# Optimization experiments

Hardware: AMD Instinct MI355X
Metric: run time of the kernel (lower is better)

The kernel has to match this reference:

```python
import jax, jax.numpy as jnp
import numpy as np

EMBED_DIM = 1024
HEAD_DIM = 64


def setup_inputs() -> dict:
    key = jax.random.key(0)
    ks = jax.random.split(key, 9)
    B, S, E, H = 4, 2048, EMBED_DIM, HEAD_DIM
    s = 1.0 / np.sqrt(E)
    return {
        "query": jax.random.normal(ks[0], (B, S, E), dtype=jnp.float32),
        "key": jax.random.normal(ks[1], (B, S, E), dtype=jnp.float32),
        "value": jax.random.normal(ks[2], (B, S, E), dtype=jnp.float32),
        "Wq": jax.random.normal(ks[3], (E, H), dtype=jnp.float32) * s,
        "bq": jnp.zeros((H,), dtype=jnp.float32),
        "Wk": jax.random.normal(ks[4], (E, H), dtype=jnp.float32) * s,
        "bk": jnp.zeros((H,), dtype=jnp.float32),
        "Wv": jax.random.normal(ks[5], (E, H), dtype=jnp.float32) * s,
        "bv": jnp.zeros((H,), dtype=jnp.float32),
    }


def reference(query, key, value, Wq, bq, Wk, bk, Wv, bv):
    # per-head linear projections: [B,S,E] @ [E,H] -> [B,S,H]
    q = jnp.einsum("bse,eh->bsh", query, Wq) + bq
    k = jnp.einsum("bse,eh->bsh", key, Wk) + bk
    v = jnp.einsum("bse,eh->bsh", value, Wv) + bv
    # NOTE: original code computes dim_k but never scales -> unscaled scores
    scores = jnp.einsum("bqh,bkh->bqk", q, k)  # [B,S,S]
    weights = jax.nn.softmax(scores, axis=-1)
    return jnp.einsum("bqk,bkh->bqh", weights, v)  # [B,S,H]
```

## Files before the change

### kernel.cpp

```cpp
#include <hip/hip_runtime.h>
#include <math.h>

#define B 4
#define S 2048
#define E 1024
#define H 64
#define BS (B*S)
#define LOG2E 1.44269504088896f
#define CINIT (-69.2493662f)

typedef float v4f __attribute__((ext_vector_type(4)));
typedef short v8s __attribute__((ext_vector_type(8)));
typedef unsigned short u16;
typedef u16 u16x8 __attribute__((ext_vector_type(8)));
typedef u16 u16x4 __attribute__((ext_vector_type(4)));

#define MFMA(a,b,c) __builtin_amdgcn_mfma_f32_16x16x32_bf16(a,b,c,0,0,0)

#define BARRIER_L() do { \
    asm volatile("s_waitcnt lgkmcnt(0)" ::: "memory"); \
    __builtin_amdgcn_s_barrier(); \
} while (0)

__device__ inline u16 rh_bf16(float x){ return (u16)((__float_as_uint(x)+0x8000u)>>16); }

__global__ __launch_bounds__(256) void wsetup_kernel(
    const float* __restrict__ Wq, const float* __restrict__ Wk,
    const float* __restrict__ Wv,
    u16* __restrict__ Wt_hi, u16* __restrict__ Wt_lo)
{
    __shared__ float wt[64][65];
    const int t  = threadIdx.x;
    const int p  = blockIdx.x >> 4;
    const int e0 = (blockIdx.x & 15) * 64;
    const float* Wsrc = (p==0) ? Wq : (p==1 ? Wk : Wv);
    const float scale = (p==0) ? LOG2E : 1.0f;

    #pragma unroll
    for (int i=0;i<16;i++){
        int e_l = i*4 + (t>>6);
        wt[e_l][t&63] = Wsrc[(size_t)(e0+e_l)*H + (t&63)] * scale;
    }
    __syncthreads();

    const int h = t>>2, e16 = (t&3)*16;
    u16 hi_a[16], lo_a[16];
    #pragma unroll
    for (int j=0;j<16;j++){
        float f = wt[e16+j][h];
        unsigned u = __float_as_uint(f);
        hi_a[j] = (u16)(u>>16);
        float hif = __uint_as_float(u & 0xFFFF0000u);
        lo_a[j] = rh_bf16(f - hif);
    }
    u16* dh = Wt_hi + (size_t)(p*64+h)*E + e0 + e16;
    u16* dl = Wt_lo + (size_t)(p*64+h)*E + e0 + e16;
    *(u16x8*)dh     = *(u16x8*)&hi_a[0];
    *(u16x8*)(dh+8) = *(u16x8*)&hi_a[8];
    *(u16x8*)dl     = *(u16x8*)&lo_a[0];
    *(u16x8*)(dl+8) = *(u16x8*)&lo_a[8];
}

__global__ __launch_bounds__(256) void proj_kernel(
    const float* __restrict__ query, const float* __restrict__ key_,
    const float* __restrict__ value,
    const u16* __restrict__ Wt_hi, const u16* __restrict__ Wt_lo,
    const float* __restrict__ bq, const float* __restrict__ bk,
    const float* __restrict__ bv,
    u16* __restrict__ q_hi, u16* __restrict__ q_lo,
    u16* __restrict__ k_hi, u16* __restrict__ k_lo,
    u16* __restrict__ vt)
{
    __shared__ __align__(16) u16 xh[32][72], xl[32][72];
    __shared__ __align__(16) u16 wh[64][72], wl[64][72];
    __shared__ __align__(16) u16 vtile[64][40];

    const int t  = threadIdx.x;
    const int p  = blockIdx.x >> 8;
    const int r0 = (blockIdx.x & 255) * 32;
    const float* xp = (p==0) ? query : (p==1 ? key_ : value);
    const int wv = t>>6, lane = t&63, m = lane&15, quad = lane>>4;
    const int whalf = wv>>1, nh = wv&1;

    const int srow = t>>3, se8 = (t&7)*8;
    const int swh  = t>>2, seo  = (t&3)*16;

    const float* xb  = xp + (size_t)(r0+srow)*E + se8;
    const u16*   shb = Wt_hi + (size_t)(p*64+swh)*E + seo;
    const u16*   slb = Wt_lo + (size_t)(p*64+swh)*E + seo;

    v4f acc[2];
    acc[0] = (v4f){0.f,0.f,0.f,0.f};
    acc[1] = (v4f){0.f,0.f,0.f,0.f};

    float4 xA[2], xB[2];
    u16x8  wA[4], wB[4];
    xA[0] = *(const float4*)(xb);
    xA[1] = *(const float4*)(xb+4);
    wA[0] = *(const u16x8*)(shb);     wA[1] = *(const u16x8*)(shb+8);
    wA[2] = *(const u16x8*)(slb);     wA[3] = *(const u16x8*)(slb+8);
    xB[0] = *(const float4*)(xb+64);
    xB[1] = *(const float4*)(xb+68);
    wB[0] = *(const u16x8*)(shb+64);  wB[1] = *(const u16x8*)(shb+72);
    wB[2] = *(const u16x8*)(slb+64);  wB[3] = *(const u16x8*)(slb+72);

#define PROJ_ITER(EC, XC, WC, PREF)                                            \
    {                                                                          \
        BARRIER_L();                                                           \
        float fv[8] = {XC[0].x,XC[0].y,XC[0].z,XC[0].w,                        \
                       XC[1].x,XC[1].y,XC[1].z,XC[1].w};                       \
        u16 ha[8], la[8];                                                      \
        _Pragma("unroll")                                                      \
        for (int j=0;j<8;j++){                                                 \
            unsigned u = __float_as_uint(fv[j]);                               \
            ha[j] = (u16)(u>>16);                                              \
            la[j] = rh_bf16(fv[j] - __uint_as_float(u & 0xFFFF0000u));         \
        }                                                                      \
        *(u16x8*)&xh[srow][se8] = *(u16x8*)&ha[0];                             \
        *(u16x8*)&xl[srow][se8] = *(u16x8*)&la[0];                             \
        *(u16x8*)&wh[swh][seo]   = WC[0];                                      \
        *(u16x8*)&wh[swh][seo+8] = WC[1];                                      \
        *(u16x8*)&wl[swh][seo]   = WC[2];                                      \
        *(u16x8*)&wl[swh][seo+8] = WC[3];                                      \
        if (PREF){                                                             \
            const float* xn = xb + ((EC)+2)*64;                                \
            XC[0] = *(const float4*)(xn);                                      \
            XC[1] = *(const float4*)(xn+4);                                    \
            const u16* shn = shb + ((EC)+2)*64;                                \
            const u16* sln = slb + ((EC)+2)*64;                                \
            WC[0]=*(const u16x8*)(shn); WC[1]=*(const u16x8*)(shn+8);          \
            WC[2]=*(const u16x8*)(sln); WC[3]=*(const u16x8*)(sln+8);          \
        }                                                                      \
        BARRIER_L();                                                           \
        v8s ah0 = *(v8s*)&xh[whalf*16+m][quad*8];                              \
        v8s ah1 = *(v8s*)&xh[whalf*16+m][32+quad*8];                           \
        v8s al0 = *(v8s*)&xl[whalf*16+m][quad*8];                              \
        v8s al1 = *(v8s*)&xl[whalf*16+m][32+quad*8];                           \
        _Pragma("unroll")                                                      \
        for (int i=0;i<2;i++){                                                 \
            const int nt = nh*2+i;                                             \
            v8s bh0 = *(v8s*)&wh[nt*16+m][quad*8];                             \
            v8s bh1 = *(v8s*)&wh[nt*16+m][32+quad*8];                          \
            v8s bl0 = *(v8s*)&wl[nt*16+m][quad*8];                             \
            v8s bl1 = *(v8s*)&wl[nt*16+m][32+quad*8];                          \
            v4f d = acc[i];                                                    \
            d = MFMA(ah0,bh0,d); d = MFMA(ah1,bh1,d);                          \
            d = MFMA(al0,bh0,d); d = MFMA(al1,bh1,d);                          \
            d = MFMA(ah0,bl0,d); d = MFMA(ah1,bl1,d);                          \
            acc[i] = d;                                                        \
        }                                                                      \
    }

    for (int ec2=0; ec2<16; ec2+=2){
        PROJ_ITER(ec2,   xA, wA, (ec2+2<16))
        PROJ_ITER(ec2+1, xB, wB, (ec2+3<16))
    }
#undef PROJ_ITER

    const float* bp = (p==0) ? bq : (p==1 ? bk : bv);
    if (p<2){
        const float bscale = (p==0) ? LOG2E : 1.0f;
        u16* dh = (p==0) ? q_hi : k_hi;
        u16* dl = (p==0) ? q_lo : k_lo;
        #pragma unroll
        for (int i=0;i<2;i++){
            const int hl = (nh*2+i)*16+m;
            const float bb = bp[hl]*bscale;
            #pragma unroll
            for (int r=0;r<4;r++){
                const int gr = r0 + whalf*16 + quad*4 + r;
                const float val = acc[i][r] + bb;
                unsigned u = __float_as_uint(val);
                u16 hi = (u16)(u>>16);
                float hif = __uint_as_float(u & 0xFFFF0000u);
                u16 lo = rh_bf16(val - hif);
                dh[(size_t)gr*H + hl] = hi;
                dl[(size_t)gr*H + hl] = lo;
            }
        }
    } else {
        const int rlb = whalf*16 + quad*4;
        #pragma unroll
        for (int i=0;i<2;i++){
            const int hl = (nh*2+i)*16+m;
            const float bb = bp[hl];
            u16 vv[4];
            #pragma unroll
            for (int r=0;r<4;r++) vv[r] = rh_bf16(acc[i][r] + bb);
            *(u16x4*)&vtile[hl][rlb] = *(u16x4*)&vv[0];
        }
        __syncthreads();
        const int h = t>>2, so = (t&3)*8;
        const int bidx = r0 >> 11, s0l = r0 & (S-1);
        u16* dst = vt + ((size_t)(bidx*H + h))*S + s0l + so;
        *(u16x8*)dst = *(const u16x8*)&vtile[h][so];
    }
}

__global__ __launch_bounds__(256) void attn_kernel(
    const u16* __restrict__ qh_g, const u16* __restrict__ ql_g,
    const u16* __restrict__ kh_g, const u16* __restrict__ kl_g,
    const u16* __restrict__ vt_g,
    float* __restrict__ accw, float* __restrict__ lw, int ksplit)
{
    __shared__ __align__(16) u16 khe[2][16][72];
    __shared__ __align__(16) u16 kle[2][16][72];
    __shared__ __align__(16) u16 vtl[64][40];
    __shared__ __align__(16) u16 pl[4][16][40];

    const int t = threadIdx.x;
    const int wv = t>>6, lane = t&63, m = lane&15, quad = lane>>4;
    const int bid = blockIdx.x;
    const int qb = bid / ksplit, chunk = bid % ksplit;
    const int b = qb >> 5, s0 = (qb & 31)*64;
    const int ck = S / ksplit;
    const int j0base = chunk * ck;
    const int iters = ck / 32;

    const u16* qr = qh_g + (size_t)(b*S + s0 + wv*16 + m)*H + quad*8;
    const u16* qrl = ql_g + (size_t)(b*S + s0 + wv*16 + m)*H + quad*8;
    const v8s qh0 = *(const v8s*)(qr),  qh1 = *(const v8s*)(qr+32);
    const v8s ql0 = *(const v8s*)(qrl), ql1 = *(const v8s*)(qrl+32);

    v4f oacc[4];
    #pragma unroll
    for (int nt=0;nt<4;nt++) oacc[nt] = (v4f){0.f,0.f,0.f,0.f};
    float lp[4] = {0.f,0.f,0.f,0.f};
    const v4f cinit = (v4f){CINIT,CINIT,CINIT,CINIT};

    const int sj = t>>3, sh8 = (t&7)*8;
    const u16* khs = kh_g + (size_t)(b*S + j0base + sj)*H + sh8;
    const u16* kls = kl_g + (size_t)(b*S + j0base + sj)*H + sh8;
    u16* khd = &khe[sj&1][sj>>1][sh8];
    u16* kld = &kle[sj&1][sj>>1][sh8];
    const int vh = t>>2, vj8 = (t&3)*8;
    const u16* vts = vt_g + (size_t)(b*H + vh)*S + j0base + vj8;
    u16* vtd = &vtl[vh][vj8];

    u16x8 khA, klA, vtA, khB, klB, vtB;
    khA = *(const u16x8*)khs;
    klA = *(const u16x8*)kls;
    vtA = *(const u16x8*)vts;
    khB = *(const u16x8*)(khs + (size_t)32*H);
    klB = *(const u16x8*)(kls + (size_t)32*H);
    vtB = *(const u16x8*)(vts + 32);

#define ATTN_ITER(IT, KHC, KLC, VTC, PREF)                                     \
    {                                                                          \
        BARRIER_L();                                                           \
        *(u16x8*)khd = KHC; *(u16x8*)kld = KLC; *(u16x8*)vtd = VTC;            \
        if (PREF){                                                             \
            KHC = *(const u16x8*)(khs + (size_t)((IT)+2)*32*H);                \
            KLC = *(const u16x8*)(kls + (size_t)((IT)+2)*32*H);                \
            VTC = *(const u16x8*)(vts + ((IT)+2)*32);                          \
        }                                                                      \
        BARRIER_L();                                                           \
                \
        v4f sc[2];                                                             \
        _Pragma("unroll")                                                      \
        for (int jt=0;jt<2;jt++){                                              \
            const u16* kr  = &khe[jt][m][quad*8];                              \
            const u16* krl = &kle[jt][m][quad*8];                              \
            v8s b0 = *(const v8s*)kr,  b1 = *(const v8s*)(kr+32);              \
            v8s c0 = *(const v8s*)krl, c1 = *(const v8s*)(krl+32);             \
            v4f d = cinit;                                                     \
            d = MFMA(qh0,b0,d); d = MFMA(qh1,b1,d);                            \
            d = MFMA(ql0,b0,d); d = MFMA(ql1,b1,d);                            \
            d = MFMA(qh0,c0,d); d = MFMA(qh1,c1,d);                            \
            sc[jt] = d;                                                        \
        }                                                                      \
            \
        _Pragma("unroll")                                                      \
        for (int r=0;r<4;r++){                                                 \
            float p0 = exp2f(sc[0][r]);                     \
            float p1 = exp2f(sc[1][r]);                     \
            lp[r] += p0 + p1;                                                  \
            unsigned pk = ((__float_as_uint(p0)+0x8000u)>>16)                  \
                        | ((__float_as_uint(p1)+0x8000u) & 0xFFFF0000u);       \
            *(unsigned*)&pl[wv][quad*4+r][2*m] = pk;                           \
        }                                                                      \
          \
        v8s pa = *(const v8s*)&pl[wv][m][quad*8];                              \
        _Pragma("unroll")                                                      \
        for (int nt=0;nt<4;nt++){                                              \
            v8s vb = *(const v8s*)&vtl[nt*16+m][quad*8];                       \
            oacc[nt] = MFMA(pa, vb, oacc[nt]);                                 \
        }                                                                      \
    }

    for (int it=0; it<iters; it+=2){
        ATTN_ITER(it,   khA,klA,vtA, (it+2<iters))
        ATTN_ITER(it+1, khB,klB,vtB, (it+3<iters))
    }
#undef ATTN_ITER

    #pragma unroll
    for (int r=0;r<4;r++){
        float v = lp[r];
        v += __shfl_xor(v,1); v += __shfl_xor(v,2);
        v += __shfl_xor(v,4); v += __shfl_xor(v,8);
        lp[r] = v;
    }
    const int growb = b*S + s0 + wv*16;
    if (m==0){
        float4 lv; lv.x=lp[0]; lv.y=lp[1]; lv.z=lp[2]; lv.w=lp[3];
        *(float4*)(lw + (size_t)chunk*BS + growb + quad*4) = lv;
    }
    float* ab = accw + ((size_t)chunk*BS + growb)*H;
    #pragma unroll
    for (int nt=0;nt<4;nt++){
        #pragma unroll
        for (int r=0;r<4;r++)
            ab[(size_t)(quad*4+r)*H + nt*16 + m] = oacc[nt][r];
    }
}

__global__ __launch_bounds__(256) void merge_kernel(
    const float* __restrict__ accw, const float* __restrict__ lw,
    float* __restrict__ out, int ksplit)
{
    const int idx = blockIdx.x*256 + threadIdx.x;
    const int row = idx >> 4, h4 = (idx & 15)*4;
    float4 a = {0.f,0.f,0.f,0.f};
    float ls = 0.f;
    for (int c=0;c<ksplit;c++){
        const float4 t4 = *(const float4*)(accw + ((size_t)c*BS + row)*H + h4);
        a.x+=t4.x; a.y+=t4.y; a.z+=t4.z; a.w+=t4.w;
        ls += lw[(size_t)c*BS + row];
    }
    const float inv = __builtin_amdgcn_rcpf(ls);
    float4 o; o.x=a.x*inv; o.y=a.y*inv; o.z=a.z*inv; o.w=a.w*inv;
    *(float4*)(out + (size_t)row*H + h4) = o;
}

extern "C" void kernel_launch(void* const* d_in, const int* in_sizes, int n_in,
                              void* d_out, int out_size, void* d_ws, size_t ws_size,
                              hipStream_t stream) {
    const float* query = (const float*)d_in[0];
    const float* key_  = (const float*)d_in[1];
    const float* value = (const float*)d_in[2];
    const float* Wq    = (const float*)d_in[3];
    const float* bq    = (const float*)d_in[4];
    const float* Wk    = (const float*)d_in[5];
    const float* bk    = (const float*)d_in[6];
    const float* Wv    = (const float*)d_in[7];
    const float* bv    = (const float*)d_in[8];
    float* out = (float*)d_out;

    char* base = (char*)d_ws;
    size_t off = 0;
    u16* Wt_hi = (u16*)(base + off); off += (size_t)3*64*E*2;
    u16* Wt_lo = (u16*)(base + off); off += (size_t)3*64*E*2;
    u16* q_hi  = (u16*)(base + off); off += (size_t)BS*H*2;
    u16* q_lo  = (u16*)(base + off); off += (size_t)BS*H*2;
    u16* k_hi  = (u16*)(base + off); off += (size_t)BS*H*2;
    u16* k_lo  = (u16*)(base + off); off += (size_t)BS*H*2;
    u16* vt    = (u16*)(base + off); off += (size_t)BS*H*2;
    const size_t fixed = off;
    const size_t CH = (size_t)BS*H*4 + (size_t)BS*4;

    int K = 1;
    if      (ws_size >= fixed + 8*CH) K = 8;
    else if (ws_size >= fixed + 4*CH) K = 4;
    else if (ws_size >= fixed + 2*CH) K = 2;

    float* lw   = (float*)(base + fixed);
    float* accw = (float*)(base + fixed + (size_t)K*BS*4);

    wsetup_kernel<<<48, 256, 0, stream>>>(Wq, Wk, Wv, Wt_hi, Wt_lo);
    proj_kernel<<<768, 256, 0, stream>>>(query, key_, value, Wt_hi, Wt_lo,
                                         bq, bk, bv, q_hi, q_lo, k_hi, k_lo, vt);
    attn_kernel<<<128*K, 256, 0, stream>>>(q_hi, q_lo, k_hi, k_lo, vt, accw, lw, K);
    merge_kernel<<<512, 256, 0, stream>>>(accw, lw, out, K);
}
```

Before: 170.1 us.

## Prepack weights in MFMA fragment order and drop LDS staging in projection

The weight setup kernel now writes Wq/Wk/Wv hi/lo bf16 splits directly in the per-lane MFMA B-fragment order. The projection kernel then loads each lane's A fragment of x straight from global memory and splits it in registers, removing the shared-memory tiles and the two barriers per K-step. Register double-buffering of x and W prefetches is kept. The cost is more registers per thread, less coalesced x loads (each wave reads 16 rows in 32-byte pieces), and each x element now being loaded by two waves.

Result: slower. 183.3 us (+7.8%).

```diff
diff --git a/kernel.cpp b/kernel.cpp
--- a/kernel.cpp
+++ b/kernel.cpp
@@ -26,13 +26,12 @@
 
 __global__ __launch_bounds__(256) void wsetup_kernel(
     const float* __restrict__ Wq, const float* __restrict__ Wk,
-    const float* __restrict__ Wv,
-    u16* __restrict__ Wt_hi, u16* __restrict__ Wt_lo)
+    const float* __restrict__ Wv, u16* __restrict__ WF)
 {
     __shared__ float wt[64][65];
     const int t  = threadIdx.x;
     const int p  = blockIdx.x >> 4;
-    const int e0 = (blockIdx.x & 15) * 64;
+    const int ec = blockIdx.x & 15, e0 = ec*64;
     const float* Wsrc = (p==0) ? Wq : (p==1 ? Wk : Wv);
     const float scale = (p==0) ? LOG2E : 1.0f;
 
@@ -43,36 +42,34 @@
     }
     __syncthreads();
 
-    const int h = t>>2, e16 = (t&3)*16;
-    u16 hi_a[16], lo_a[16];
-    #pragma unroll
-    for (int j=0;j<16;j++){
-        float f = wt[e16+j][h];
-        unsigned u = __float_as_uint(f);
-        hi_a[j] = (u16)(u>>16);
-        float hif = __uint_as_float(u & 0xFFFF0000u);
-        lo_a[j] = rh_bf16(f - hif);
-    }
-    u16* dh = Wt_hi + (size_t)(p*64+h)*E + e0 + e16;
-    u16* dl = Wt_lo + (size_t)(p*64+h)*E + e0 + e16;
-    *(u16x8*)dh     = *(u16x8*)&hi_a[0];
-    *(u16x8*)(dh+8) = *(u16x8*)&hi_a[8];
-    *(u16x8*)dl     = *(u16x8*)&lo_a[0];
-    *(u16x8*)(dl+8) = *(u16x8*)&lo_a[8];
+    u16* dst = WF + (((size_t)(p*16 + ec))*1024 + (size_t)t*4)*8;
+    #pragma unroll
+    for (int k=0;k<4;k++){
+        const int c   = t*4 + k;
+        const int l   = c & 63, b01 = (c>>6)&1, pl = (c>>7)&1, nt = c>>8;
+        const int m   = l & 15, quad = l>>4;
+        u16 o8[8];
+        #pragma unroll
+        for (int j=0;j<8;j++){
+            float f = wt[b01*32 + quad*8 + j][nt*16 + m];
+            unsigned u = __float_as_uint(f);
+            if (pl==0) o8[j] = (u16)(u>>16);
+            else       o8[j] = rh_bf16(f - __uint_as_float(u & 0xFFFF0000u));
+        }
+        *(u16x8*)(dst + (size_t)k*8) = *(u16x8*)&o8[0];
+    }
 }
 
 __global__ __launch_bounds__(256) void proj_kernel(
     const float* __restrict__ query, const float* __restrict__ key_,
     const float* __restrict__ value,
-    const u16* __restrict__ Wt_hi, const u16* __restrict__ Wt_lo,
+    const u16* __restrict__ WF,
     const float* __restrict__ bq, const float* __restrict__ bk,
     const float* __restrict__ bv,
     u16* __restrict__ q_hi, u16* __restrict__ q_lo,
     u16* __restrict__ k_hi, u16* __restrict__ k_lo,
     u16* __restrict__ vt)
 {
-    __shared__ __align__(16) u16 xh[32][72], xl[32][72];
-    __shared__ __align__(16) u16 wh[64][72], wl[64][72];
     __shared__ __align__(16) u16 vtile[64][40];
 
     const int t  = threadIdx.x;
@@ -82,82 +79,74 @@
     const int wv = t>>6, lane = t&63, m = lane&15, quad = lane>>4;
     const int whalf = wv>>1, nh = wv&1;
 
-    const int srow = t>>3, se8 = (t&7)*8;
-    const int swh  = t>>2, seo  = (t&3)*16;
-
-    const float* xb  = xp + (size_t)(r0+srow)*E + se8;
-    const u16*   shb = Wt_hi + (size_t)(p*64+swh)*E + seo;
-    const u16*   slb = Wt_lo + (size_t)(p*64+swh)*E + seo;
-
-    v4f acc[2];
-    acc[0] = (v4f){0.f,0.f,0.f,0.f};
-    acc[1] = (v4f){0.f,0.f,0.f,0.f};
-
-    float4 xA[2], xB[2];
-    u16x8  wA[4], wB[4];
-    xA[0] = *(const float4*)(xb);
-    xA[1] = *(const float4*)(xb+4);
-    wA[0] = *(const u16x8*)(shb);     wA[1] = *(const u16x8*)(shb+8);
-    wA[2] = *(const u16x8*)(slb);     wA[3] = *(const u16x8*)(slb+8);
-    xB[0] = *(const float4*)(xb+64);
-    xB[1] = *(const float4*)(xb+68);
-    wB[0] = *(const u16x8*)(shb+64);  wB[1] = *(const u16x8*)(shb+72);
-    wB[2] = *(const u16x8*)(slb+64);  wB[3] = *(const u16x8*)(slb+72);
-
-#define PROJ_ITER(EC, XC, WC, PREF)                                            \
-    {                                                                          \
-        BARRIER_L();                                                           \
-        float fv[8] = {XC[0].x,XC[0].y,XC[0].z,XC[0].w,                        \
-                       XC[1].x,XC[1].y,XC[1].z,XC[1].w};                       \
-        u16 ha[8], la[8];                                                      \
+    const float* xr = xp + (size_t)(r0 + whalf*16 + m)*E + quad*8;
+    const u16* wfb = WF + (size_t)p*131072 + (size_t)nh*4096 + (size_t)lane*8;
+
+    v4f acc0 = (v4f){0.f,0.f,0.f,0.f};
+    v4f acc1 = (v4f){0.f,0.f,0.f,0.f};
+
+#define LOADX(X, EC) {                                                         \
+        const float* xa = xr + (size_t)(EC)*64;                                \
+        X[0] = *(const float4*)(xa);                                           \
+        X[1] = *(const float4*)(xa+4);                                         \
+        X[2] = *(const float4*)(xa+32);                                        \
+        X[3] = *(const float4*)(xa+36);                                        \
+    }
+#define LOADW(W, EC) {                                                         \
+        const u16* wb = wfb + (size_t)(EC)*8192;                               \
+        W[0] = *(const v8s*)(wb);                                              \
+        W[1] = *(const v8s*)(wb+512);                                          \
+        W[2] = *(const v8s*)(wb+1024);                                         \
+        W[3] = *(const v8s*)(wb+1536);                                         \
+        W[4] = *(const v8s*)(wb+2048);                                         \
+        W[5] = *(const v8s*)(wb+2560);                                         \
+        W[6] = *(const v8s*)(wb+3072);                                         \
+        W[7] = *(const v8s*)(wb+3584);                                         \
+    }
+#define COMPUTE(X, W) {                                                        \
+        float fv[16] = {X[0].x,X[0].y,X[0].z,X[0].w,                           \
+                        X[1].x,X[1].y,X[1].z,X[1].w,                           \
+                        X[2].x,X[2].y,X[2].z,X[2].w,                           \
+                        X[3].x,X[3].y,X[3].z,X[3].w};                          \
+        u16 ha[16], la[16];                                                    \
         _Pragma("unroll")                                                      \
-        for (int j=0;j<8;j++){                                                 \
+        for (int j=0;j<16;j++){                                                \
             unsigned u = __float_as_uint(fv[j]);                               \
             ha[j] = (u16)(u>>16);                                              \
             la[j] = rh_bf16(fv[j] - __uint_as_float(u & 0xFFFF0000u));         \
         }                                                                      \
-        *(u16x8*)&xh[srow][se8] = *(u16x8*)&ha[0];                             \
-        *(u16x8*)&xl[srow][se8] = *(u16x8*)&la[0];                             \
-        *(u16x8*)&wh[swh][seo]   = WC[0];                                      \
-        *(u16x8*)&wh[swh][seo+8] = WC[1];                                      \
-        *(u16x8*)&wl[swh][seo]   = WC[2];                                      \
-        *(u16x8*)&wl[swh][seo+8] = WC[3];                                      \
-        if (PREF){                                                             \
-            const float* xn = xb + ((EC)+2)*64;                                \
-            XC[0] = *(const float4*)(xn);                                      \
-            XC[1] = *(const float4*)(xn+4);                                    \
-            const u16* shn = shb + ((EC)+2)*64;                                \
-            const u16* sln = slb + ((EC)+2)*64;                                \
-            WC[0]=*(const u16x8*)(shn); WC[1]=*(const u16x8*)(shn+8);          \
-            WC[2]=*(const u16x8*)(sln); WC[3]=*(const u16x8*)(sln+8);          \
-        }                                                                      \
-        BARRIER_L();                                                           \
-        v8s ah0 = *(v8s*)&xh[whalf*16+m][quad*8];                              \
-        v8s ah1 = *(v8s*)&xh[whalf*16+m][32+quad*8];                           \
-        v8s al0 = *(v8s*)&xl[whalf*16+m][quad*8];                              \
-        v8s al1 = *(v8s*)&xl[whalf*16+m][32+quad*8];                           \
-        _Pragma("unroll")                                                      \
-        for (int i=0;i<2;i++){                                                 \
-            const int nt = nh*2+i;                                             \
-            v8s bh0 = *(v8s*)&wh[nt*16+m][quad*8];                             \
-            v8s bh1 = *(v8s*)&wh[nt*16+m][32+quad*8];                          \
-            v8s bl0 = *(v8s*)&wl[nt*16+m][quad*8];                             \
-            v8s bl1 = *(v8s*)&wl[nt*16+m][32+quad*8];                          \
-            v4f d = acc[i];                                                    \
-            d = MFMA(ah0,bh0,d); d = MFMA(ah1,bh1,d);                          \
-            d = MFMA(al0,bh0,d); d = MFMA(al1,bh1,d);                          \
-            d = MFMA(ah0,bl0,d); d = MFMA(ah1,bl1,d);                          \
-            acc[i] = d;                                                        \
-        }                                                                      \
-    }
-
+        v8s ah0 = *(v8s*)&ha[0], ah1 = *(v8s*)&ha[8];                          \
+        v8s al0 = *(v8s*)&la[0], al1 = *(v8s*)&la[8];                          \
+        v4f d0 = acc0;                                                         \
+        d0 = MFMA(ah0,W[0],d0); d0 = MFMA(ah1,W[1],d0);                        \
+        d0 = MFMA(al0,W[0],d0); d0 = MFMA(al1,W[1],d0);                        \
+        d0 = MFMA(ah0,W[2],d0); d0 = MFMA(ah1,W[3],d0);                        \
+        acc0 = d0;                                                             \
+        v4f d1 = acc1;                                                         \
+        d1 = MFMA(ah0,W[4],d1); d1 = MFMA(ah1,W[5],d1);                        \
+        d1 = MFMA(al0,W[4],d1); d1 = MFMA(al1,W[5],d1);                        \
+        d1 = MFMA(ah0,W[6],d1); d1 = MFMA(ah1,W[7],d1);                        \
+        acc1 = d1;                                                             \
+    }
+
+    float4 xA[4], xB[4];
+    v8s    wA[8], wB[8];
+    LOADX(xA, 0); LOADW(wA, 0);
+    LOADX(xB, 1); LOADW(wB, 1);
+
+    #pragma unroll
     for (int ec2=0; ec2<16; ec2+=2){
-        PROJ_ITER(ec2,   xA, wA, (ec2+2<16))
-        PROJ_ITER(ec2+1, xB, wB, (ec2+3<16))
-    }
-#undef PROJ_ITER
+        COMPUTE(xA, wA);
+        if (ec2+2<16){ LOADX(xA, ec2+2); LOADW(wA, ec2+2); }
+        COMPUTE(xB, wB);
+        if (ec2+3<16){ LOADX(xB, ec2+3); LOADW(wB, ec2+3); }
+    }
+#undef LOADX
+#undef LOADW
+#undef COMPUTE
 
     const float* bp = (p==0) ? bq : (p==1 ? bk : bv);
+    v4f accv[2]; accv[0] = acc0; accv[1] = acc1;
     if (p<2){
         const float bscale = (p==0) ? LOG2E : 1.0f;
         u16* dh = (p==0) ? q_hi : k_hi;
@@ -169,7 +158,7 @@
             #pragma unroll
             for (int r=0;r<4;r++){
                 const int gr = r0 + whalf*16 + quad*4 + r;
-                const float val = acc[i][r] + bb;
+                const float val = accv[i][r] + bb;
                 unsigned u = __float_as_uint(val);
                 u16 hi = (u16)(u>>16);
                 float hif = __uint_as_float(u & 0xFFFF0000u);
@@ -186,7 +175,7 @@
             const float bb = bp[hl];
             u16 vv[4];
             #pragma unroll
-            for (int r=0;r<4;r++) vv[r] = rh_bf16(acc[i][r] + bb);
+            for (int r=0;r<4;r++) vv[r] = rh_bf16(accv[i][r] + bb);
             *(u16x4*)&vtile[hl][rlb] = *(u16x4*)&vv[0];
         }
         __syncthreads();
@@ -349,8 +338,7 @@
 
     char* base = (char*)d_ws;
     size_t off = 0;
-    u16* Wt_hi = (u16*)(base + off); off += (size_t)3*64*E*2;
-    u16* Wt_lo = (u16*)(base + off); off += (size_t)3*64*E*2;
+    u16* WF    = (u16*)(base + off); off += (size_t)3*16*1024*8*2;
     u16* q_hi  = (u16*)(base + off); off += (size_t)BS*H*2;
     u16* q_lo  = (u16*)(base + off); off += (size_t)BS*H*2;
     u16* k_hi  = (u16*)(base + off); off += (size_t)BS*H*2;
@@ -367,8 +355,8 @@
     float* lw   = (float*)(base + fixed);
     float* accw = (float*)(base + fixed + (size_t)K*BS*4);
 
-    wsetup_kernel<<<48, 256, 0, stream>>>(Wq, Wk, Wv, Wt_hi, Wt_lo);
-    proj_kernel<<<768, 256, 0, stream>>>(query, key_, value, Wt_hi, Wt_lo,
+    wsetup_kernel<<<48, 256, 0, stream>>>(Wq, Wk, Wv, WF);
+    proj_kernel<<<768, 256, 0, stream>>>(query, key_, value, WF,
                                          bq, bk, bv, q_hi, q_lo, k_hi, k_lo, vt);
     attn_kernel<<<128*K, 256, 0, stream>>>(q_hi, q_lo, k_hi, k_lo, vt, accw, lw, K);
     merge_kernel<<<512, 256, 0, stream>>>(accw, lw, out, K);
```
